# Kernel optimization log

Hardware: AMD Instinct MI355X
Metric: run time of the kernel (lower is better)

## Reference

```python
import jax, jax.numpy as jnp
import numpy as np

FEAT_DIM = 256
NUM_HEADS = 4
GATE_HID = FEAT_DIM // 4
LN_EPS = 1e-5


def setup_inputs() -> dict:
    key = jax.random.key(0)
    ks = jax.random.split(key, 12)
    C, H = FEAT_DIM, NUM_HEADS
    s = 1.0 / np.sqrt(C)
    inp = {
        "features": jax.random.normal(ks[0], (8, 16384, C), dtype=jnp.float32),
        "view_proj_w": jax.random.normal(ks[1], (C, C), dtype=jnp.float32) * s,
        "view_proj_b": jnp.zeros((C,), dtype=jnp.float32),
        "in_proj_w": jax.random.normal(ks[2], (3 * C, C), dtype=jnp.float32) * s,
        "in_proj_b": jnp.zeros((3 * C,), dtype=jnp.float32),
        "out_proj_w": jax.random.normal(ks[3], (C, C), dtype=jnp.float32) * s,
        "out_proj_b": jnp.zeros((C,), dtype=jnp.float32),
        "gate_w1": jax.random.normal(ks[4], (GATE_HID, C), dtype=jnp.float32) * s,
        "gate_b1": jnp.zeros((GATE_HID,), dtype=jnp.float32),
        "gate_w2": jax.random.normal(ks[5], (1, GATE_HID), dtype=jnp.float32) * (1.0 / np.sqrt(GATE_HID)),
        "gate_b2": jnp.zeros((1,), dtype=jnp.float32),
        "ln_g": jnp.ones((C,), dtype=jnp.float32),
        "ln_b": jnp.zeros((C,), dtype=jnp.float32),
    }
    return inp


def reference(features, view_proj_w, view_proj_b, in_proj_w, in_proj_b,
              out_proj_w, out_proj_b, gate_w1, gate_b1, gate_w2, gate_b2,
              ln_g, ln_b):
    N, L, C = features.shape
    H = NUM_HEADS
    D = C // H

    # view embedding: scalar id/N broadcast over C, then Linear  -> [N,1,C]
    view_ids = (jnp.arange(N, dtype=features.dtype) / N)[:, None, None]  # [N,1,1]
    view_vec = jnp.broadcast_to(view_ids, (N, 1, C))
    view_info = view_vec @ view_proj_w.T + view_proj_b                    # [N,1,C]
    view_features = features + view_info                                  # [N,L,C]

    tokens = jnp.transpose(view_features, (1, 0, 2))                      # [L,N,C]

    # batched tiny cross-view self-attention: batch=L, seq=N
    qkv = tokens @ in_proj_w.T + in_proj_b                                # [L,N,3C]
    q, k, v = jnp.split(qkv, 3, axis=-1)
    q = q.reshape(L, N, H, D)
    k = k.reshape(L, N, H, D)
    v = v.reshape(L, N, H, D)
    scores = jnp.einsum("lnhd,lmhd->lhnm", q, k) / jnp.sqrt(jnp.array(D, features.dtype))
    attn = jax.nn.softmax(scores, axis=-1)                                # [L,H,N,N]
    ctx = jnp.einsum("lhnm,lmhd->lnhd", attn, v).reshape(L, N, C)
    attended = ctx @ out_proj_w.T + out_proj_b                            # [L,N,C]

    # gated softmax aggregation over views
    g = jax.nn.relu(attended @ gate_w1.T + gate_b1)                       # [L,N,C/4]
    g = jax.nn.sigmoid(g @ gate_w2.T + gate_b2)[..., 0]                   # [L,N]
    w = jax.nn.softmax(g, axis=-1)                                        # [L,N]
    fused = jnp.einsum("lnc,ln->lc", attended, w)[None]                   # [1,L,C]

    # LayerNorm over C
    mu = fused.mean(-1, keepdims=True)
    var = fused.var(-1, keepdims=True)
    fused = (fused - mu) * jax.lax.rsqrt(var + LN_EPS) * ln_g + ln_b
    return fused
```

## Files before the change

### kernel.cpp

```cpp
#include <hip/hip_runtime.h>

#define L_DIM 16384
#define C_DIM 256
#define NV 8
#define NH 4
#define DH 64
#define TL 4
#define NTHREADS 256

#define QKP 132
#define VVP 68
#define GPAD 65

typedef __attribute__((ext_vector_type(8))) _Float16 f16x8;
typedef __attribute__((ext_vector_type(4))) float f32x4;

__global__ void prep_kernel(const float* __restrict__ vw, const float* __restrict__ vb,
                            const float* __restrict__ w_in, const float* __restrict__ w_out,
                            const float* __restrict__ w_g1,
                            float* __restrict__ view_info, _Float16* __restrict__ win_pk,
                            _Float16* __restrict__ wout_pk, _Float16* __restrict__ wg1_pk){
  int tid = threadIdx.x, bid = blockIdx.x;
  if (bid == 0){
    int c = tid;
    const float4* vr = (const float4*)(vw + c*C_DIM);
    float rs = 0.f;
#pragma unroll 8
    for (int k = 0; k < 64; k++){ float4 x = vr[k]; rs += x.x + x.y + x.z + x.w; }
    float b = vb[c];
    for (int n = 0; n < NV; n++) view_info[n*C_DIM + c] = (n * 0.125f) * rs + b;
  }
  int gid = bid * blockDim.x + tid;
  int stride = gridDim.x * blockDim.x;
  const int NWIN = 24576, NWOUT = 8192, NWG = 2048;
  for (int f = gid; f < NWIN + NWOUT + NWG; f += stride){
    if (f < NWIN){
      int lane = f & 63, kc = (f>>6)&7, nt = (f>>9)&3, pc = f>>11;
      int p = pc % 3, h = pc / 3;
      int row = p*C_DIM + h*DH + nt*16 + (lane&15);
      int col = (lane>>4)*8 + kc*32;
      const float* src = w_in + (long)row*C_DIM + col;
      _Float16* d = win_pk + (long)f*8;
#pragma unroll
      for (int j = 0; j < 8; j++) d[j] = (_Float16)src[j];
    } else if (f < NWIN + NWOUT){
      int f2 = f - NWIN;
      int lane = f2 & 63, kc = (f2>>6)&7, nt = (f2>>9)&3, cc = f2>>11;
      int row = cc*64 + nt*16 + (lane&15);
      int col = (lane>>4)*8 + kc*32;
      const float* src = w_out + (long)row*C_DIM + col;
      _Float16* d = wout_pk + (long)f2*8;
#pragma unroll
      for (int j = 0; j < 8; j++) d[j] = (_Float16)src[j];
    } else {
      int f3 = f - NWIN - NWOUT;
      int lane = f3 & 63, kc = (f3>>6)&7, nt = (f3>>9)&3;
      int row = nt*16 + (lane&15);
      int col = (lane>>4)*8 + kc*32;
      const float* src = w_g1 + (long)row*C_DIM + col;
      _Float16* d = wg1_pk + (long)f3*8;
#pragma unroll
      for (int j = 0; j < 8; j++) d[j] = (_Float16)src[j];
    }
  }
}

__global__ __launch_bounds__(NTHREADS, 3)
void fused_kernel(const float* __restrict__ feat,
                  const float* __restrict__ view_info,
                  const _Float16* __restrict__ win,
                  const _Float16* __restrict__ wout,
                  const _Float16* __restrict__ wg1,
                  const float* __restrict__ b_in,
                  const float* __restrict__ b_out,
                  const float* __restrict__ b_g1,
                  const float* __restrict__ w2,
                  const float* __restrict__ b2,
                  const float* __restrict__ ln_g,
                  const float* __restrict__ ln_b,
                  float* __restrict__ out)
{
  extern __shared__ char smem[];
  _Float16* A   = (_Float16*)smem;
  _Float16* att = (_Float16*)smem;
  _Float16* qk  = (_Float16*)(smem + 16384);
  float*    g1s = (float*)(smem + 16384);
  _Float16* vv  = (_Float16*)(smem + 24832);
  _Float16* ctx = (_Float16*)(smem + 29184);
  float* gl   = (float*)(smem + 45568);
  float* wgt  = gl + 32;
  float* red1 = wgt + 32;
  float* red2 = red1 + 128;
  float* mus  = red2 + 128;
  float* rvs  = mus + 4;

  const int tid  = threadIdx.x;
  const int wv   = tid >> 6, lane = tid & 63;
  const int quad = lane >> 4, l15 = lane & 15;

  {
    int row = tid >> 3, j = tid & 7;
    int n = row & 7, lloc = row >> 3;
    long l = (long)blockIdx.x * TL + lloc;
    const float* fb = feat + ((long)n * L_DIM + l) * C_DIM + j*32;
    const float* vb = view_info + n * C_DIM + j*32;
    _Float16* arow = A + row*256;
#pragma unroll
    for (int i = 0; i < 4; i++){
      float4 x0 = *(const float4*)(fb + i*8);
      float4 x1 = *(const float4*)(fb + i*8 + 4);
      float4 v0 = *(const float4*)(vb + i*8);
      float4 v1 = *(const float4*)(vb + i*8 + 4);
      f16x8 hf;
      hf[0] = (_Float16)(x0.x+v0.x); hf[1] = (_Float16)(x0.y+v0.y);
      hf[2] = (_Float16)(x0.z+v0.z); hf[3] = (_Float16)(x0.w+v0.w);
      hf[4] = (_Float16)(x1.x+v1.x); hf[5] = (_Float16)(x1.y+v1.y);
      hf[6] = (_Float16)(x1.z+v1.z); hf[7] = (_Float16)(x1.w+v1.w);
      int s = j*4 + i;
      *(f16x8*)(arow + ((s ^ row))*8) = hf;
    }
  }
  __syncthreads();

  for (int h = 0; h < NH; h++){
    if (h) __syncthreads();
    {
      const _Float16* bp = win + (long)(h*96 + wv*8)*512 + lane*8;
      f32x4 z = {0.f,0.f,0.f,0.f};
      f32x4 acc[3][2];
#pragma unroll
      for (int p = 0; p < 3; p++){ acc[p][0] = z; acc[p][1] = z; }
#pragma unroll
      for (int kc = 0; kc < 8; kc++){
        int s0 = quad + 4*kc;
        int r1 = 16 + l15;
        f16x8 a0 = *(const f16x8*)(A + l15*256 + ((s0 ^ l15))*8);
        f16x8 a1 = *(const f16x8*)(A + r1*256  + ((s0 ^ r1))*8);
#pragma unroll
        for (int p = 0; p < 3; p++){
          f16x8 b = *(const f16x8*)(bp + (p*32 + kc)*512);
          acc[p][0] = __builtin_amdgcn_mfma_f32_16x16x32_f16(a0, b, acc[p][0], 0,0,0);
          acc[p][1] = __builtin_amdgcn_mfma_f32_16x16x32_f16(a1, b, acc[p][1], 0,0,0);
        }
      }
      int colc = wv*16 + l15;
#pragma unroll
      for (int p = 0; p < 2; p++){
        float bias = b_in[p*C_DIM + h*DH + colc];
#pragma unroll
        for (int r = 0; r < 4; r++){
          qk[(quad*4 + r)*QKP + p*64 + colc]      = (_Float16)(acc[p][0][r] + bias);
          qk[(16 + quad*4 + r)*QKP + p*64 + colc] = (_Float16)(acc[p][1][r] + bias);
        }
      }
      {
        float bias = b_in[2*C_DIM + h*DH + colc];
#pragma unroll
        for (int r = 0; r < 4; r++){
          vv[(quad*4 + r)*VVP + colc]      = (_Float16)(acc[2][0][r] + bias);
          vv[(16 + quad*4 + r)*VVP + colc] = (_Float16)(acc[2][1][r] + bias);
        }
      }
    }
    __syncthreads();
    {
      int nn = lane >> 3, mm = lane & 7;
      int tq = wv*8 + nn;
      const _Float16* qrow = qk + tq*QKP;
      const _Float16* krow = qk + (wv*8 + mm)*QKP + 64;
      float s = 0.f;
#pragma unroll
      for (int d8 = 0; d8 < 8; d8++){
        f16x8 q8 = *(const f16x8*)(qrow + d8*8);
        f16x8 k8 = *(const f16x8*)(krow + d8*8);
#pragma unroll
        for (int j = 0; j < 8; j++) s += (float)q8[j] * (float)k8[j];
      }
      s *= 0.125f;
      float mx = s;
#pragma unroll
      for (int o = 1; o < 8; o <<= 1) mx = fmaxf(mx, __shfl_xor(mx, o));
      float e = __expf(s - mx);
      float sum = e;
#pragma unroll
      for (int o = 1; o < 8; o <<= 1) sum += __shfl_xor(sum, o);
      float attnw = e / sum;
      float c8[8] = {0,0,0,0,0,0,0,0};
#pragma unroll
      for (int mp = 0; mp < 8; mp++){
        float aw = __shfl(attnw, (nn<<3) | mp);
        f16x8 v8 = *(const f16x8*)(vv + (wv*8 + mp)*VVP + mm*8);
#pragma unroll
        for (int j = 0; j < 8; j++) c8[j] += aw * (float)v8[j];
      }
      f16x8 cp;
#pragma unroll
      for (int j = 0; j < 8; j++) cp[j] = (_Float16)c8[j];
      int slot = h*8 + mm;
      *(f16x8*)(ctx + tq*256 + ((slot ^ (tq & 31)))*8) = cp;
    }
  }
  __syncthreads();

  {
    f32x4 z = {0.f,0.f,0.f,0.f};
    f32x4 acc[4][2];
#pragma unroll
    for (int nt = 0; nt < 4; nt++){ acc[nt][0] = z; acc[nt][1] = z; }
#pragma unroll
    for (int kc = 0; kc < 8; kc++){
      int s0 = quad + 4*kc;
      int r1 = 16 + l15;
      f16x8 a0 = *(const f16x8*)(ctx + l15*256 + ((s0 ^ l15))*8);
      f16x8 a1 = *(const f16x8*)(ctx + r1*256  + ((s0 ^ r1))*8);
#pragma unroll
      for (int nt = 0; nt < 4; nt++){
        f16x8 b = *(const f16x8*)(wout + (long)((wv*32 + nt*8 + kc)*512) + lane*8);
        acc[nt][0] = __builtin_amdgcn_mfma_f32_16x16x32_f16(a0, b, acc[nt][0], 0,0,0);
        acc[nt][1] = __builtin_amdgcn_mfma_f32_16x16x32_f16(a1, b, acc[nt][1], 0,0,0);
      }
    }
#pragma unroll
    for (int nt = 0; nt < 4; nt++){
      int col = wv*64 + nt*16 + l15;
      float bias = b_out[col];
      int slot = col >> 3, j = col & 7;
#pragma unroll
      for (int r = 0; r < 4; r++){
        int row0 = quad*4 + r, row1 = 16 + quad*4 + r;
        att[row0*256 + ((slot ^ row0))*8 + j] = (_Float16)(acc[nt][0][r] + bias);
        att[row1*256 + ((slot ^ row1))*8 + j] = (_Float16)(acc[nt][1][r] + bias);
      }
    }
  }
  __syncthreads();

  {
    f32x4 acc0 = {0.f,0.f,0.f,0.f}, acc1 = {0.f,0.f,0.f,0.f};
#pragma unroll
    for (int kc = 0; kc < 8; kc++){
      int s0 = quad + 4*kc;
      int r1 = 16 + l15;
      f16x8 a0 = *(const f16x8*)(att + l15*256 + ((s0 ^ l15))*8);
      f16x8 a1 = *(const f16x8*)(att + r1*256  + ((s0 ^ r1))*8);
      f16x8 b = *(const f16x8*)(wg1 + (long)((wv*8 + kc)*512) + lane*8);
      acc0 = __builtin_amdgcn_mfma_f32_16x16x32_f16(a0, b, acc0, 0,0,0);
      acc1 = __builtin_amdgcn_mfma_f32_16x16x32_f16(a1, b, acc1, 0,0,0);
    }
    int col = wv*16 + l15;
    float bias = b_g1[col];
#pragma unroll
    for (int r = 0; r < 4; r++){
      g1s[(quad*4 + r)*GPAD + col]      = fmaxf(acc0[r] + bias, 0.f);
      g1s[(16 + quad*4 + r)*GPAD + col] = fmaxf(acc1[r] + bias, 0.f);
    }
  }
  __syncthreads();

  {
    int t = tid >> 3, part = tid & 7;
    const float* g1r = g1s + t*GPAD + part*8;
    const float* w2p = w2 + part*8;
    float s = 0.f;
#pragma unroll
    for (int j = 0; j < 8; j++) s += g1r[j] * w2p[j];
    s += __shfl_xor(s, 1);
    s += __shfl_xor(s, 2);
    s += __shfl_xor(s, 4);
    if (part == 0) gl[t] = 1.f / (1.f + __expf(-(s + b2[0])));
  }
  __syncthreads();
  if (tid < 4){
    float v[8]; float mx = -1e30f;
    for (int n = 0; n < 8; n++){ v[n] = gl[tid*8+n]; mx = fmaxf(mx, v[n]); }
    float sum = 0.f;
    for (int n = 0; n < 8; n++){ v[n] = __expf(v[n]-mx); sum += v[n]; }
    float inv = 1.f/sum;
    for (int n = 0; n < 8; n++) wgt[tid*8+n] = v[n]*inv;
  }
  __syncthreads();

  float f8[8];
  const int lfl = tid >> 5, ccf = tid & 31;
  if (tid < 128){
    float wloc[8];
#pragma unroll
    for (int n = 0; n < 8; n++) wloc[n] = wgt[lfl*8+n];
#pragma unroll
    for (int j = 0; j < 8; j++) f8[j] = 0.f;
#pragma unroll
    for (int n = 0; n < 8; n++){
      int row = lfl*8 + n;
      f16x8 a8 = *(const f16x8*)(att + row*256 + ((ccf ^ row))*8);
      float aw = wloc[n];
#pragma unroll
      for (int j = 0; j < 8; j++) f8[j] += aw * (float)a8[j];
    }
    float s = 0.f, s2 = 0.f;
#pragma unroll
    for (int j = 0; j < 8; j++){ s += f8[j]; s2 += f8[j]*f8[j]; }
    red1[lfl*32 + ccf] = s;
    red2[lfl*32 + ccf] = s2;
  }
  __syncthreads();
  if (tid < 4){
    float s = 0.f, s2 = 0.f;
    for (int i = 0; i < 32; i++){ s += red1[tid*32+i]; s2 += red2[tid*32+i]; }
    float mu = s * (1.f/256.f);
    float var = s2 * (1.f/256.f) - mu*mu;
    mus[tid] = mu;
    rvs[tid] = rsqrtf(var + 1e-5f);
  }
  __syncthreads();
  if (tid < 128){
    float mu = mus[lfl], rv = rvs[lfl];
    long lg = (long)blockIdx.x * TL + lfl;
    float* op = out + lg * C_DIM + ccf*8;
    float o8[8];
#pragma unroll
    for (int j = 0; j < 8; j++){
      int c = ccf*8 + j;
      o8[j] = (f8[j]-mu)*rv*ln_g[c] + ln_b[c];
    }
    *(float4*)(op)   = make_float4(o8[0],o8[1],o8[2],o8[3]);
    *(float4*)(op+4) = make_float4(o8[4],o8[5],o8[6],o8[7]);
  }
}

extern "C" void kernel_launch(void* const* d_in, const int* in_sizes, int n_in,
                              void* d_out, int out_size, void* d_ws, size_t ws_size,
                              hipStream_t stream){
  const float* feat  = (const float*)d_in[0];
  const float* vw    = (const float*)d_in[1];
  const float* vb    = (const float*)d_in[2];
  const float* w_in  = (const float*)d_in[3];
  const float* b_in  = (const float*)d_in[4];
  const float* w_out = (const float*)d_in[5];
  const float* b_out = (const float*)d_in[6];
  const float* w_g1  = (const float*)d_in[7];
  const float* b_g1  = (const float*)d_in[8];
  const float* w2    = (const float*)d_in[9];
  const float* b2    = (const float*)d_in[10];
  const float* lng   = (const float*)d_in[11];
  const float* lnb   = (const float*)d_in[12];

  char* ws = (char*)d_ws;
  float*    view_info = (float*)ws;
  _Float16* win_pk  = (_Float16*)(ws + 8192);
  _Float16* wout_pk = (_Float16*)(ws + 401408);
  _Float16* wg1_pk  = (_Float16*)(ws + 532480);

  prep_kernel<<<256, 256, 0, stream>>>(vw, vb, w_in, w_out, w_g1,
                                       view_info, win_pk, wout_pk, wg1_pk);
  fused_kernel<<<L_DIM/TL, NTHREADS, 46880, stream>>>(
      feat, view_info, win_pk, wout_pk, wg1_pk,
      b_in, b_out, b_g1, w2, b2, lng, lnb, (float*)d_out);
}
```

Before: 487.8 us.

## Shrink LDS footprint, prefetch weight fragments, use fdot2 for attention scores

Per-head context fragments are held in registers until the last head and written to LDS once, so ctx can alias the input tile. The LDS layout is compacted so dynamic shared memory drops from about 46.9KB to 34KB, and launch bounds rise to allow four blocks per CU. The B-operand weight loads in all three MFMA GEMMs are software-prefetched one k-step ahead, and the QK dot products use packed fp16 fdot2. The trade-off is more register pressure under a tighter launch bound, which could cause spills, plus an extra barrier before att is written.

```diff
diff --git a/kernel.cpp b/kernel.cpp
--- a/kernel.cpp
+++ b/kernel.cpp
@@ -13,7 +13,10 @@
 #define GPAD 65
 
 typedef __attribute__((ext_vector_type(8))) _Float16 f16x8;
+typedef __attribute__((ext_vector_type(2))) _Float16 f16x2;
 typedef __attribute__((ext_vector_type(4))) float f32x4;
+
+union F8u { f16x8 v; f16x2 p[4]; };
 
 __global__ void prep_kernel(const float* __restrict__ vw, const float* __restrict__ vb,
                             const float* __restrict__ w_in, const float* __restrict__ w_out,
@@ -65,7 +68,7 @@
   }
 }
 
-__global__ __launch_bounds__(NTHREADS, 3)
+__global__ __launch_bounds__(NTHREADS, 4)
 void fused_kernel(const float* __restrict__ feat,
                   const float* __restrict__ view_info,
                   const _Float16* __restrict__ win,
@@ -82,12 +85,12 @@
 {
   extern __shared__ char smem[];
   _Float16* A   = (_Float16*)smem;
-  _Float16* att = (_Float16*)smem;
+  _Float16* ctx = (_Float16*)smem;
+  float*    g1s = (float*)smem;
   _Float16* qk  = (_Float16*)(smem + 16384);
-  float*    g1s = (float*)(smem + 16384);
   _Float16* vv  = (_Float16*)(smem + 24832);
-  _Float16* ctx = (_Float16*)(smem + 29184);
-  float* gl   = (float*)(smem + 45568);
+  _Float16* att = (_Float16*)(smem + 16384);
+  float* gl   = (float*)(smem + 32768);
   float* wgt  = gl + 32;
   float* red1 = wgt + 32;
   float* red2 = red1 + 128;
@@ -122,43 +125,60 @@
   }
   __syncthreads();
 
+  f16x8 cpk0, cpk1, cpk2;
+#pragma unroll
   for (int h = 0; h < NH; h++){
     if (h) __syncthreads();
     {
       const _Float16* bp = win + (long)(h*96 + wv*8)*512 + lane*8;
       f32x4 z = {0.f,0.f,0.f,0.f};
-      f32x4 acc[3][2];
-#pragma unroll
-      for (int p = 0; p < 3; p++){ acc[p][0] = z; acc[p][1] = z; }
+      f32x4 acc00=z, acc01=z, acc10=z, acc11=z, acc20=z, acc21=z;
+      f16x8 bq0 = *(const f16x8*)(bp);
+      f16x8 bq1 = *(const f16x8*)(bp + 32*512);
+      f16x8 bq2 = *(const f16x8*)(bp + 64*512);
 #pragma unroll
       for (int kc = 0; kc < 8; kc++){
+        f16x8 bn0, bn1, bn2;
+        if (kc < 7){
+          bn0 = *(const f16x8*)(bp + (kc+1)*512);
+          bn1 = *(const f16x8*)(bp + (32+kc+1)*512);
+          bn2 = *(const f16x8*)(bp + (64+kc+1)*512);
+        }
         int s0 = quad + 4*kc;
         int r1 = 16 + l15;
         f16x8 a0 = *(const f16x8*)(A + l15*256 + ((s0 ^ l15))*8);
         f16x8 a1 = *(const f16x8*)(A + r1*256  + ((s0 ^ r1))*8);
-#pragma unroll
-        for (int p = 0; p < 3; p++){
-          f16x8 b = *(const f16x8*)(bp + (p*32 + kc)*512);
-          acc[p][0] = __builtin_amdgcn_mfma_f32_16x16x32_f16(a0, b, acc[p][0], 0,0,0);
-          acc[p][1] = __builtin_amdgcn_mfma_f32_16x16x32_f16(a1, b, acc[p][1], 0,0,0);
+        acc00 = __builtin_amdgcn_mfma_f32_16x16x32_f16(a0, bq0, acc00, 0,0,0);
+        acc01 = __builtin_amdgcn_mfma_f32_16x16x32_f16(a1, bq0, acc01, 0,0,0);
+        acc10 = __builtin_amdgcn_mfma_f32_16x16x32_f16(a0, bq1, acc10, 0,0,0);
+        acc11 = __builtin_amdgcn_mfma_f32_16x16x32_f16(a1, bq1, acc11, 0,0,0);
+        acc20 = __builtin_amdgcn_mfma_f32_16x16x32_f16(a0, bq2, acc20, 0,0,0);
+        acc21 = __builtin_amdgcn_mfma_f32_16x16x32_f16(a1, bq2, acc21, 0,0,0);
+        bq0 = bn0; bq1 = bn1; bq2 = bn2;
+      }
+      int colc = wv*16 + l15;
+      {
+        float bias = b_in[h*DH + colc];
+#pragma unroll
+        for (int r = 0; r < 4; r++){
+          qk[(quad*4 + r)*QKP + colc]      = (_Float16)(acc00[r] + bias);
+          qk[(16 + quad*4 + r)*QKP + colc] = (_Float16)(acc01[r] + bias);
         }
       }
-      int colc = wv*16 + l15;
-#pragma unroll
-      for (int p = 0; p < 2; p++){
-        float bias = b_in[p*C_DIM + h*DH + colc];
+      {
+        float bias = b_in[C_DIM + h*DH + colc];
 #pragma unroll
         for (int r = 0; r < 4; r++){
-          qk[(quad*4 + r)*QKP + p*64 + colc]      = (_Float16)(acc[p][0][r] + bias);
-          qk[(16 + quad*4 + r)*QKP + p*64 + colc] = (_Float16)(acc[p][1][r] + bias);
+          qk[(quad*4 + r)*QKP + 64 + colc]      = (_Float16)(acc10[r] + bias);
+          qk[(16 + quad*4 + r)*QKP + 64 + colc] = (_Float16)(acc11[r] + bias);
         }
       }
       {
         float bias = b_in[2*C_DIM + h*DH + colc];
 #pragma unroll
         for (int r = 0; r < 4; r++){
-          vv[(quad*4 + r)*VVP + colc]      = (_Float16)(acc[2][0][r] + bias);
-          vv[(16 + quad*4 + r)*VVP + colc] = (_Float16)(acc[2][1][r] + bias);
+          vv[(quad*4 + r)*VVP + colc]      = (_Float16)(acc20[r] + bias);
+          vv[(16 + quad*4 + r)*VVP + colc] = (_Float16)(acc21[r] + bias);
         }
       }
     }
@@ -171,10 +191,17 @@
       float s = 0.f;
 #pragma unroll
       for (int d8 = 0; d8 < 8; d8++){
-        f16x8 q8 = *(const f16x8*)(qrow + d8*8);
-        f16x8 k8 = *(const f16x8*)(krow + d8*8);
-#pragma unroll
-        for (int j = 0; j < 8; j++) s += (float)q8[j] * (float)k8[j];
+        F8u q8, k8;
+        q8.v = *(const f16x8*)(qrow + d8*8);
+        k8.v = *(const f16x8*)(krow + d8*8);
+#if __has_builtin(__builtin_amdgcn_fdot2)
+#pragma unroll
+        for (int j2 = 0; j2 < 4; j2++)
+          s = __builtin_amdgcn_fdot2(q8.p[j2], k8.p[j2], s, false);
+#else
+#pragma unroll
+        for (int j = 0; j < 8; j++) s += (float)q8.v[j] * (float)k8.v[j];
+#endif
       }
       s *= 0.125f;
       float mx = s;
@@ -196,8 +223,16 @@
       f16x8 cp;
 #pragma unroll
       for (int j = 0; j < 8; j++) cp[j] = (_Float16)c8[j];
-      int slot = h*8 + mm;
-      *(f16x8*)(ctx + tq*256 + ((slot ^ (tq & 31)))*8) = cp;
+      if (h == 0)      cpk0 = cp;
+      else if (h == 1) cpk1 = cp;
+      else if (h == 2) cpk2 = cp;
+      else {
+        _Float16* crow = ctx + tq*256;
+        *(f16x8*)(crow + ((( 0 + mm) ^ tq))*8) = cpk0;
+        *(f16x8*)(crow + ((( 8 + mm) ^ tq))*8) = cpk1;
+        *(f16x8*)(crow + (((16 + mm) ^ tq))*8) = cpk2;
+        *(f16x8*)(crow + (((24 + mm) ^ tq))*8) = cp;
+      }
     }
   }
   __syncthreads();
@@ -207,19 +242,30 @@
     f32x4 acc[4][2];
 #pragma unroll
     for (int nt = 0; nt < 4; nt++){ acc[nt][0] = z; acc[nt][1] = z; }
+    const _Float16* bp = wout + (long)(wv*32)*512 + lane*8;
+    f16x8 bq[4], bn[4];
+#pragma unroll
+    for (int nt = 0; nt < 4; nt++) bq[nt] = *(const f16x8*)(bp + (nt*8)*512);
 #pragma unroll
     for (int kc = 0; kc < 8; kc++){
+      if (kc < 7){
+#pragma unroll
+        for (int nt = 0; nt < 4; nt++)
+          bn[nt] = *(const f16x8*)(bp + (nt*8 + kc + 1)*512);
+      }
       int s0 = quad + 4*kc;
       int r1 = 16 + l15;
       f16x8 a0 = *(const f16x8*)(ctx + l15*256 + ((s0 ^ l15))*8);
       f16x8 a1 = *(const f16x8*)(ctx + r1*256  + ((s0 ^ r1))*8);
 #pragma unroll
       for (int nt = 0; nt < 4; nt++){
-        f16x8 b = *(const f16x8*)(wout + (long)((wv*32 + nt*8 + kc)*512) + lane*8);
-        acc[nt][0] = __builtin_amdgcn_mfma_f32_16x16x32_f16(a0, b, acc[nt][0], 0,0,0);
-        acc[nt][1] = __builtin_amdgcn_mfma_f32_16x16x32_f16(a1, b, acc[nt][1], 0,0,0);
-      }
-    }
+        acc[nt][0] = __builtin_amdgcn_mfma_f32_16x16x32_f16(a0, bq[nt], acc[nt][0], 0,0,0);
+        acc[nt][1] = __builtin_amdgcn_mfma_f32_16x16x32_f16(a1, bq[nt], acc[nt][1], 0,0,0);
+      }
+#pragma unroll
+      for (int nt = 0; nt < 4; nt++) bq[nt] = bn[nt];
+    }
+    __syncthreads();
 #pragma unroll
     for (int nt = 0; nt < 4; nt++){
       int col = wv*64 + nt*16 + l15;
@@ -237,15 +283,19 @@
 
   {
     f32x4 acc0 = {0.f,0.f,0.f,0.f}, acc1 = {0.f,0.f,0.f,0.f};
+    const _Float16* bp = wg1 + (long)(wv*8)*512 + lane*8;
+    f16x8 bq = *(const f16x8*)(bp);
 #pragma unroll
     for (int kc = 0; kc < 8; kc++){
+      f16x8 bn;
+      if (kc < 7) bn = *(const f16x8*)(bp + (kc+1)*512);
       int s0 = quad + 4*kc;
       int r1 = 16 + l15;
       f16x8 a0 = *(const f16x8*)(att + l15*256 + ((s0 ^ l15))*8);
       f16x8 a1 = *(const f16x8*)(att + r1*256  + ((s0 ^ r1))*8);
-      f16x8 b = *(const f16x8*)(wg1 + (long)((wv*8 + kc)*512) + lane*8);
-      acc0 = __builtin_amdgcn_mfma_f32_16x16x32_f16(a0, b, acc0, 0,0,0);
-      acc1 = __builtin_amdgcn_mfma_f32_16x16x32_f16(a1, b, acc1, 0,0,0);
+      acc0 = __builtin_amdgcn_mfma_f32_16x16x32_f16(a0, bq, acc0, 0,0,0);
+      acc1 = __builtin_amdgcn_mfma_f32_16x16x32_f16(a1, bq, acc1, 0,0,0);
+      bq = bn;
     }
     int col = wv*16 + l15;
     float bias = b_g1[col];
@@ -352,7 +402,7 @@
 
   prep_kernel<<<256, 256, 0, stream>>>(vw, vb, w_in, w_out, w_g1,
                                        view_info, win_pk, wout_pk, wg1_pk);
-  fused_kernel<<<L_DIM/TL, NTHREADS, 46880, stream>>>(
+  fused_kernel<<<L_DIM/TL, NTHREADS, 34080, stream>>>(
       feat, view_info, win_pk, wout_pk, wg1_pk,
       b_in, b_out, b_g1, w2, b2, lng, lnb, (float*)d_out);
 }
```

After: 431.1 us. -11.6%, faster.
